# Kernel optimization log

Measured on AMD Instinct MI355X. Metric: run time of the kernel, lower is better.

The kernel has to match this reference:

```python
import jax, jax.numpy as jnp
import numpy as np

SIZE = 48          # grid edge
DIST = 4           # local neighborhood edge
PAD = DIST // 2    # padding = 2
PADDED = SIZE + 2 * PAD  # 52
RATE = 5           # recurrent steps
CONVEY = 0.9
N_IN = 2048        # input injection sites


def setup_inputs() -> dict:
    key = jax.random.key(0)
    ks = jax.random.split(key, 8)
    neuron_matrix = jnp.zeros((PADDED, PADDED, PADDED), dtype=jnp.float32)
    vinput = jax.random.normal(ks[0], (N_IN,), dtype=jnp.float32)
    # scale synapse so the 5-step relu recurrence stays numerically tame
    synapse = jax.random.normal(ks[1], (SIZE, SIZE, SIZE, DIST, DIST, DIST), dtype=jnp.float32) * 0.05
    W1 = jax.random.normal(ks[2], (SIZE ** 3, 1024), dtype=jnp.float32) * (1.0 / np.sqrt(SIZE ** 3))
    b1 = jnp.zeros((1024,), dtype=jnp.float32)
    W2 = jax.random.normal(ks[3], (1024, 128), dtype=jnp.float32) * (1.0 / np.sqrt(1024))
    b2 = jnp.zeros((128,), dtype=jnp.float32)
    W3 = jax.random.normal(ks[4], (128, 10), dtype=jnp.float32) * (1.0 / np.sqrt(128))
    b3 = jnp.zeros((10,), dtype=jnp.float32)
    node_idx = jax.random.randint(ks[5], (N_IN, 3), 0, SIZE)  # interior coords
    return {"neuron_matrix": neuron_matrix, "vinput": vinput, "synapse": synapse,
            "W1": W1, "b1": b1, "W2": W2, "b2": b2, "W3": W3, "b3": b3,
            "node_idx": node_idx}


def _windows(p):
    # p: [PADDED]^3 -> sliding DxDxD windows at every interior site: [S,S,S,D,D,D]
    idx = jnp.arange(SIZE)[:, None] + jnp.arange(DIST)[None, :]  # [S, D]
    w = jnp.take(p, idx, axis=0)   # [S, D, P, P]
    w = jnp.take(w, idx, axis=2)   # [S, D, S, D, P]
    w = jnp.take(w, idx, axis=4)   # [S, D, S, D, S, D]
    return jnp.transpose(w, (0, 2, 4, 1, 3, 5))  # [S, S, S, D, D, D]


def reference(neuron_matrix, vinput, synapse, W1, b1, W2, b2, W3, b3, node_idx):
    # inject inputs at (possibly colliding) interior nodes (scatter-add, like +=)
    nm = neuron_matrix.at[node_idx[:, 0] + PAD,
                          node_idx[:, 1] + PAD,
                          node_idx[:, 2] + PAD].add(vinput)
    # recurrent locally-connected 3D neighbor aggregation, RATE steps
    for _ in range(RATE):
        win = _windows(nm)  # [S,S,S,D,D,D]
        agg = jnp.einsum('xyzabc,xyzabc->xyz', synapse, win)  # per-site unique-weight reduce
        interior = jax.nn.relu(agg) * CONVEY
        nm = jnp.pad(interior, PAD)  # re-pad with zeros for next step
    x = interior.reshape(1, SIZE ** 3)
    x = jax.nn.relu(x @ W1 + b1)
    x = jax.nn.relu(x @ W2 + b2)
    return x @ W3 + b3  # [1, 10]
```

## Files before the change

### kernel.cpp

```cpp
#include <hip/hip_runtime.h>

#define S 48
#define D 4
#define PADC 2
#define P 52
#define SITES (S * S * S)
#define PADVOL (P * P * P)
#define N_IN 2048
#define H1 1024
#define H2 128
#define OUTN 10
#define RP 64
#define NCH (SITES / RP)
#define RG 16
#define CHPG (NCH / RG)
#define G2B 32

__global__ __launch_bounds__(256) void zero_k(float4* __restrict__ p, int n4) {
    int i = blockIdx.x * 256 + threadIdx.x;
    if (i < n4) p[i] = make_float4(0.f, 0.f, 0.f, 0.f);
}

__global__ void scatter_k(const float* __restrict__ vin,
                          const int* __restrict__ idx,
                          float* __restrict__ nm) {
    int t = blockIdx.x * blockDim.x + threadIdx.x;
    if (t < N_IN) {
        int x = idx[t * 3 + 0] + PADC;
        int y = idx[t * 3 + 1] + PADC;
        int z = idx[t * 3 + 2] + PADC;
        atomicAdd(&nm[(x * P + y) * P + z], vin[t]);
    }
}

__global__ __launch_bounds__(256) void step_k(const float* __restrict__ src,
                                              const float* __restrict__ syn,
                                              float* __restrict__ dst) {
    int tid = threadIdx.x;
    int q = tid & 3;
    int sl = tid >> 2;
    int s = blockIdx.x * 64 + sl;
    int z = s % S;
    int t2 = s / S;
    int y = t2 % S;
    int x = t2 / S;
    const float4* sv = (const float4*)(syn + (size_t)s * 64);
    float acc = 0.0f;
#pragma unroll
    for (int a = 0; a < D; a++) {
        const float* row = src + ((x + a) * P + (y + q)) * P + z;
        float4 w = sv[a * 4 + q];
        acc += w.x * row[0] + w.y * row[1] + w.z * row[2] + w.w * row[3];
    }
    acc += __shfl_xor(acc, 1);
    acc += __shfl_xor(acc, 2);
    if (q == 0) {
        dst[((x + PADC) * P + (y + PADC)) * P + (z + PADC)] = fmaxf(acc, 0.0f) * 0.9f;
    }
}

__global__ __launch_bounds__(256) void gemv1_k(const float* __restrict__ nmfin,
                                               const float* __restrict__ W1,
                                               float* __restrict__ partial) {
    int t = threadIdx.x;
    int lane = t & 63;
    int i0 = blockIdx.x * RP;

    int i = i0 + lane;
    int z = i % S;
    int q = i / S;
    int y = q % S;
    int x = q / S;
    float v = nmfin[((x + PADC) * P + (y + PADC)) * P + (z + PADC)];
    unsigned long long mask = __ballot(v != 0.0f);

    const float4* W4 = (const float4*)W1;
    size_t base = (size_t)i0 * (H1 / 4) + t;
    float4 a0 = {0.f, 0.f, 0.f, 0.f};
    float4 a1 = {0.f, 0.f, 0.f, 0.f};
    float4 a2 = {0.f, 0.f, 0.f, 0.f};
    float4 a3 = {0.f, 0.f, 0.f, 0.f};
    int nnz = __popcll(mask);
    for (int k = 0; k + 4 <= nnz; k += 4) {
        int r0 = (int)__builtin_ctzll(mask); mask &= mask - 1;
        int r1 = (int)__builtin_ctzll(mask); mask &= mask - 1;
        int r2 = (int)__builtin_ctzll(mask); mask &= mask - 1;
        int r3 = (int)__builtin_ctzll(mask); mask &= mask - 1;
        float x0 = __int_as_float(__builtin_amdgcn_readlane(__float_as_int(v), r0));
        float x1 = __int_as_float(__builtin_amdgcn_readlane(__float_as_int(v), r1));
        float x2 = __int_as_float(__builtin_amdgcn_readlane(__float_as_int(v), r2));
        float x3 = __int_as_float(__builtin_amdgcn_readlane(__float_as_int(v), r3));
        float4 w0 = W4[base + (size_t)r0 * (H1 / 4)];
        float4 w1 = W4[base + (size_t)r1 * (H1 / 4)];
        float4 w2 = W4[base + (size_t)r2 * (H1 / 4)];
        float4 w3 = W4[base + (size_t)r3 * (H1 / 4)];
        a0.x += x0 * w0.x; a0.y += x0 * w0.y; a0.z += x0 * w0.z; a0.w += x0 * w0.w;
        a1.x += x1 * w1.x; a1.y += x1 * w1.y; a1.z += x1 * w1.z; a1.w += x1 * w1.w;
        a2.x += x2 * w2.x; a2.y += x2 * w2.y; a2.z += x2 * w2.z; a2.w += x2 * w2.w;
        a3.x += x3 * w3.x; a3.y += x3 * w3.y; a3.z += x3 * w3.z; a3.w += x3 * w3.w;
    }
    while (mask) {
        int r0 = (int)__builtin_ctzll(mask); mask &= mask - 1;
        float x0 = __int_as_float(__builtin_amdgcn_readlane(__float_as_int(v), r0));
        float4 w0 = W4[base + (size_t)r0 * (H1 / 4)];
        a0.x += x0 * w0.x; a0.y += x0 * w0.y; a0.z += x0 * w0.z; a0.w += x0 * w0.w;
    }
    float4 acc = {a0.x + a1.x + a2.x + a3.x,
                  a0.y + a1.y + a2.y + a3.y,
                  a0.z + a1.z + a2.z + a3.z,
                  a0.w + a1.w + a2.w + a3.w};
    ((float4*)(partial + (size_t)blockIdx.x * H1))[t] = acc;
}

__global__ __launch_bounds__(256) void reduceA_k(const float* __restrict__ partial,
                                                 float* __restrict__ redB) {
    int g = blockIdx.x >> 2;
    int c = (blockIdx.x & 3) * 256 + threadIdx.x;
    float s = 0.0f;
    int r0 = g * CHPG;
#pragma unroll 4
    for (int r = r0; r < r0 + CHPG; r++) s += partial[(size_t)r * H1 + c];
    redB[g * H1 + c] = s;
}

__global__ __launch_bounds__(128) void gemv2_k(const float* __restrict__ redB,
                                               const float* __restrict__ b1,
                                               const float* __restrict__ W2,
                                               float* __restrict__ partial2) {
    __shared__ float ys[H1 / G2B];
    int b = blockIdx.x;
    int t = threadIdx.x;
    int r0 = b * (H1 / G2B);
    if (t < H1 / G2B) {
        int j = r0 + t;
        float s = b1[j];
#pragma unroll
        for (int g = 0; g < RG; g++) s += redB[g * H1 + j];
        ys[t] = fmaxf(s, 0.0f);
    }
    __syncthreads();
    float acc = 0.0f;
#pragma unroll
    for (int i = 0; i < H1 / G2B; i++)
        acc += ys[i] * W2[(size_t)(r0 + i) * H2 + t];
    partial2[b * H2 + t] = acc;
}

__global__ __launch_bounds__(128) void final_k(const float* __restrict__ partial2,
                                               const float* __restrict__ b2,
                                               const float* __restrict__ W3,
                                               const float* __restrict__ b3,
                                               float* __restrict__ out) {
    __shared__ float y2[H2];
    int t = threadIdx.x;
    float s = b2[t];
#pragma unroll
    for (int k = 0; k < G2B; k++) s += partial2[k * H2 + t];
    y2[t] = fmaxf(s, 0.0f);
    __syncthreads();
    if (t < OUTN) {
        float o = b3[t];
#pragma unroll 8
        for (int i = 0; i < H2; i++) o += y2[i] * W3[i * OUTN + t];
        out[t] = o;
    }
}

extern "C" void kernel_launch(void* const* d_in, const int* in_sizes, int n_in,
                              void* d_out, int out_size, void* d_ws, size_t ws_size,
                              hipStream_t stream) {
    const float* vinput  = (const float*)d_in[1];
    const float* synapse = (const float*)d_in[2];
    const float* W1      = (const float*)d_in[3];
    const float* b1      = (const float*)d_in[4];
    const float* W2      = (const float*)d_in[5];
    const float* b2      = (const float*)d_in[6];
    const float* W3      = (const float*)d_in[7];
    const float* b3      = (const float*)d_in[8];
    const int* node_idx  = (const int*)d_in[9];

    float* ws = (float*)d_ws;
    float* nm0 = ws;
    float* nm1 = nm0 + PADVOL;
    float* partial1 = nm1 + PADVOL;
    float* redB = partial1 + (size_t)NCH * H1;
    float* partial2 = redB + RG * H1;
    float* out = (float*)d_out;

    const int n4 = 2 * PADVOL / 4;
    zero_k<<<(n4 + 255) / 256, 256, 0, stream>>>((float4*)nm0, n4);

    scatter_k<<<N_IN / 256, 256, 0, stream>>>(vinput, node_idx, nm0);

    const float* src = nm0;
    float* dst = nm1;
    for (int r = 0; r < 5; r++) {
        step_k<<<SITES / 64, 256, 0, stream>>>(src, synapse, dst);
        float* tmp = (float*)src;
        src = dst;
        dst = tmp;
    }

    gemv1_k<<<NCH, 256, 0, stream>>>(src, W1, partial1);
    reduceA_k<<<RG * 4, 256, 0, stream>>>(partial1, redB);
    gemv2_k<<<G2B, 128, 0, stream>>>(redB, b1, W2, partial2);
    final_k<<<1, 128, 0, stream>>>(partial2, b2, W3, b3, out);
}
```

Baseline: 92.03 us.

## Fuse last recurrent step into W1 GEMV and fold final layer via last-block counter

The fifth stencil step is computed directly inside the first GEMV kernel, so its output no longer needs a separate launch or a write and read through global memory. In that kernel every lane of all four wavefronts recomputes the same 64-term site reduction, which adds redundant work and synapse reads. The final small layer is folded into the second GEMV using an atomic arrival counter, reset in the zero kernel; the last block to arrive sums the partials and writes the output, removing another launch.

```diff
diff --git a/kernel.cpp b/kernel.cpp
--- a/kernel.cpp
+++ b/kernel.cpp
@@ -16,9 +16,11 @@
 #define CHPG (NCH / RG)
 #define G2B 32
 
-__global__ __launch_bounds__(256) void zero_k(float4* __restrict__ p, int n4) {
+__global__ __launch_bounds__(256) void zero_k(float4* __restrict__ p, int n4,
+                                              int* __restrict__ cnt) {
     int i = blockIdx.x * 256 + threadIdx.x;
     if (i < n4) p[i] = make_float4(0.f, 0.f, 0.f, 0.f);
+    if (i == 0) *cnt = 0;
 }
 
 __global__ void scatter_k(const float* __restrict__ vin,
@@ -59,19 +61,31 @@
     }
 }
 
-__global__ __launch_bounds__(256) void gemv1_k(const float* __restrict__ nmfin,
-                                               const float* __restrict__ W1,
-                                               float* __restrict__ partial) {
+__global__ __launch_bounds__(256) void gemv1f_k(const float* __restrict__ src,
+                                                const float* __restrict__ syn,
+                                                const float* __restrict__ W1,
+                                                float* __restrict__ partial) {
     int t = threadIdx.x;
     int lane = t & 63;
     int i0 = blockIdx.x * RP;
 
-    int i = i0 + lane;
-    int z = i % S;
-    int q = i / S;
+    int s = i0 + lane;
+    int z = s % S;
+    int q = s / S;
     int y = q % S;
     int x = q / S;
-    float v = nmfin[((x + PADC) * P + (y + PADC)) * P + (z + PADC)];
+    const float4* sv = (const float4*)(syn + (size_t)s * 64);
+    float sum = 0.0f;
+#pragma unroll
+    for (int a = 0; a < D; a++) {
+#pragma unroll
+        for (int b = 0; b < D; b++) {
+            const float* row = src + ((x + a) * P + (y + b)) * P + z;
+            float4 w = sv[a * 4 + b];
+            sum += w.x * row[0] + w.y * row[1] + w.z * row[2] + w.w * row[3];
+        }
+    }
+    float v = fmaxf(sum, 0.0f) * 0.9f;
     unsigned long long mask = __ballot(v != 0.0f);
 
     const float4* W4 = (const float4*)W1;
@@ -123,11 +137,17 @@
     redB[g * H1 + c] = s;
 }
 
-__global__ __launch_bounds__(128) void gemv2_k(const float* __restrict__ redB,
-                                               const float* __restrict__ b1,
-                                               const float* __restrict__ W2,
-                                               float* __restrict__ partial2) {
+__global__ __launch_bounds__(128) void gemv2f_k(const float* __restrict__ redB,
+                                                const float* __restrict__ b1,
+                                                const float* __restrict__ W2,
+                                                const float* __restrict__ b2,
+                                                const float* __restrict__ W3,
+                                                const float* __restrict__ b3,
+                                                float* __restrict__ partial2,
+                                                int* __restrict__ cnt,
+                                                float* __restrict__ out) {
     __shared__ float ys[H1 / G2B];
+    __shared__ int amlast;
     int b = blockIdx.x;
     int t = threadIdx.x;
     int r0 = b * (H1 / G2B);
@@ -144,25 +164,28 @@
     for (int i = 0; i < H1 / G2B; i++)
         acc += ys[i] * W2[(size_t)(r0 + i) * H2 + t];
     partial2[b * H2 + t] = acc;
-}
-
-__global__ __launch_bounds__(128) void final_k(const float* __restrict__ partial2,
-                                               const float* __restrict__ b2,
-                                               const float* __restrict__ W3,
-                                               const float* __restrict__ b3,
-                                               float* __restrict__ out) {
-    __shared__ float y2[H2];
-    int t = threadIdx.x;
-    float s = b2[t];
-#pragma unroll
-    for (int k = 0; k < G2B; k++) s += partial2[k * H2 + t];
-    y2[t] = fmaxf(s, 0.0f);
+
+    __threadfence();
     __syncthreads();
-    if (t < OUTN) {
-        float o = b3[t];
+    if (t == 0) {
+        int prev = atomicAdd(cnt, 1);
+        amlast = (prev == G2B - 1) ? 1 : 0;
+    }
+    __syncthreads();
+    if (amlast) {
+        __threadfence();
+        __shared__ float y2[H2];
+        float s2 = b2[t];
+#pragma unroll
+        for (int k = 0; k < G2B; k++) s2 += partial2[k * H2 + t];
+        y2[t] = fmaxf(s2, 0.0f);
+        __syncthreads();
+        if (t < OUTN) {
+            float o = b3[t];
 #pragma unroll 8
-        for (int i = 0; i < H2; i++) o += y2[i] * W3[i * OUTN + t];
-        out[t] = o;
+            for (int k = 0; k < H2; k++) o += y2[k] * W3[k * OUTN + t];
+            out[t] = o;
+        }
     }
 }
 
@@ -185,24 +208,25 @@
     float* partial1 = nm1 + PADVOL;
     float* redB = partial1 + (size_t)NCH * H1;
     float* partial2 = redB + RG * H1;
+    int* cnt = (int*)(partial2 + G2B * H2);
     float* out = (float*)d_out;
 
     const int n4 = 2 * PADVOL / 4;
-    zero_k<<<(n4 + 255) / 256, 256, 0, stream>>>((float4*)nm0, n4);
+    zero_k<<<(n4 + 255) / 256, 256, 0, stream>>>((float4*)nm0, n4, cnt);
 
     scatter_k<<<N_IN / 256, 256, 0, stream>>>(vinput, node_idx, nm0);
 
     const float* src = nm0;
     float* dst = nm1;
-    for (int r = 0; r < 5; r++) {
+    for (int r = 0; r < 4; r++) {
         step_k<<<SITES / 64, 256, 0, stream>>>(src, synapse, dst);
         float* tmp = (float*)src;
         src = dst;
         dst = tmp;
     }
 
-    gemv1_k<<<NCH, 256, 0, stream>>>(src, W1, partial1);
+    gemv1f_k<<<NCH, 256, 0, stream>>>(src, synapse, W1, partial1);
     reduceA_k<<<RG * 4, 256, 0, stream>>>(partial1, redB);
-    gemv2_k<<<G2B, 128, 0, stream>>>(redB, b1, W2, partial2);
-    final_k<<<1, 128, 0, stream>>>(partial2, b2, W3, b3, out);
-}
+    gemv2f_k<<<G2B, 128, 0, stream>>>(redB, b1, W2, b2, W3, b3,
+                                      partial2, cnt, out);
+}
```

Result: slower. 99.81 us (+8.5%).
